# Kernel tuning notes

Hardware: AMD Instinct MI355X
Metric: run time of the kernel (lower is better)

The kernel has to match this reference:

```python
import jax, jax.numpy as jnp
import numpy as np

B, S, D = 8, 512, 1024
E, F, K = 8, 4096, 2


def setup_inputs() -> dict:
    key = jax.random.key(0)
    ks = jax.random.split(key, 8)
    scale = 1.0 / np.sqrt(D)
    return {
        "x": jax.random.normal(ks[0], (B, S, D), jnp.float32),
        "y": jax.random.randint(ks[1], (B,), 0, D),
        "W": jax.random.normal(ks[2], (D, D), jnp.float32) * scale,
        "b": jnp.zeros((D,), jnp.float32),
        "Wg": jax.random.normal(ks[3], (D, E), jnp.float32) * scale,
        "w1": jax.random.normal(ks[4], (E, D, F), jnp.float32) * scale,
        "b1": jnp.zeros((E, F), jnp.float32),
        "w2": jax.random.normal(ks[5], (E, F, D), jnp.float32) * (1.0 / np.sqrt(F)),
        "b2": jnp.zeros((E, D), jnp.float32),
    }


def reference(x, y, W, b, Wg, w1, b1, w2, b2):
    # linear projection (torch Linear convention: x @ W.T + b)
    lin = jnp.einsum("bsd,ed->bse", x, W) + b                      # [B,S,D]

    # --- MoE: top-2 softmax gate, renormalized over the top-k ---
    gate_logits = jnp.einsum("bsd,de->bse", lin, Wg)               # [B,S,E]
    probs = jax.nn.softmax(gate_logits, axis=-1)
    top_p, top_i = jax.lax.top_k(probs, K)                          # [B,S,K]
    top_p = top_p / jnp.sum(top_p, axis=-1, keepdims=True)
    # combine weights per expert: scatter top-k probs back to [B,S,E]
    gate = jnp.sum(jax.nn.one_hot(top_i, E, dtype=lin.dtype) * top_p[..., None], axis=-2)  # [B,S,E]

    # expert FFNs evaluated densely, combined by (sparse) gate weights
    h = jax.nn.relu(jnp.einsum("bsd,edf->ebsf", lin, w1) + b1[:, None, None, :])  # [E,B,S,F]
    expert_out = jnp.einsum("ebsf,efd->ebsd", h, w2) + b2[:, None, None, :]        # [E,B,S,D]
    moe_out = jnp.einsum("bse,ebsd->bsd", gate, expert_out)                        # [B,S,D]

    # residual, mean pool over sequence, cross-entropy
    sent_emb = jnp.mean(x + moe_out, axis=1)                       # [B,D] used as logits
    logp = jax.nn.log_softmax(sent_emb, axis=-1)
    loss = -jnp.mean(logp[jnp.arange(B), y])
    return loss
```

## Files before the change

kernel.cpp:

```cpp
#include <hip/hip_runtime.h>

#define TOK 4096
#define DD  1024
#define NE  8
#define FF  4096
#define NB  8
#define SS  512
#define HROWS 8320

typedef unsigned short ushort_t;
typedef __attribute__((ext_vector_type(8))) short bshort8;
typedef __attribute__((ext_vector_type(4))) float floatx4;

__device__ __forceinline__ ushort_t f2bf(float f) {
  unsigned int u = __float_as_uint(f);
  u += 0x7fffu + ((u >> 16) & 1u);
  return (ushort_t)(u >> 16);
}
__device__ __forceinline__ float bf2f(ushort_t h) {
  return __uint_as_float(((unsigned int)h) << 16);
}

__device__ __forceinline__ void gl_lds16(const ushort_t* g, ushort_t* l) {
  __builtin_amdgcn_global_load_lds(
      (const __attribute__((address_space(1))) unsigned int*)g,
      (__attribute__((address_space(3))) unsigned int*)l, 16, 0, 0);
}

__global__ __launch_bounds__(256) void k_cast(
    const float* __restrict__ in, ushort_t* __restrict__ out, int n4) {
  int i = blockIdx.x * 256 + threadIdx.x;
  if (i < n4) {
    float4 v = ((const float4*)in)[i];
    ushort4 o;
    o.x = f2bf(v.x); o.y = f2bf(v.y); o.z = f2bf(v.z); o.w = f2bf(v.w);
    ((ushort4*)out)[i] = o;
  }
}

__global__ __launch_bounds__(256) void k_transpose_cast(
    const float* __restrict__ in, size_t in_estride, int in_rstride,
    ushort_t* __restrict__ out, size_t out_estride, int out_rstride) {
  __shared__ ushort_t t[64][70];
  const float* ib = in + blockIdx.z * in_estride;
  ushort_t* ob = out + blockIdx.z * out_estride;
  const int r0 = blockIdx.y * 64, c0 = blockIdx.x * 64;
  const int tid = threadIdx.x;
  const int lr = tid >> 4, lc4 = (tid & 15) * 4;
#pragma unroll
  for (int it = 0; it < 4; ++it) {
    int r = lr + it * 16;
    float4 v = *(const float4*)&ib[(size_t)(r0 + r) * in_rstride + c0 + lc4];
    t[r][lc4 + 0] = f2bf(v.x);
    t[r][lc4 + 1] = f2bf(v.y);
    t[r][lc4 + 2] = f2bf(v.z);
    t[r][lc4 + 3] = f2bf(v.w);
  }
  __syncthreads();
  const int oc = tid >> 5, od2 = (tid & 31) * 2;
#pragma unroll
  for (int it = 0; it < 8; ++it) {
    int cc = oc + it * 8;
    ushort2 w;
    w.x = t[od2 + 0][cc];
    w.y = t[od2 + 1][cc];
    *(ushort2*)&ob[(size_t)(c0 + cc) * out_rstride + r0 + od2] = w;
  }
}

template <int MODE>
__global__ __launch_bounds__(256) void k_mfma(
    const ushort_t* __restrict__ A, const ushort_t* __restrict__ Bm,
    const float* __restrict__ bias, ushort_t* __restrict__ Obf,
    float* __restrict__ Of, const int* __restrict__ cnt,
    const int* __restrict__ offs, const int* __restrict__ btok, int f0,
    int accum, int kext, int ast, int ost, size_t bstride) {
  const int gx = gridDim.x, gy = gridDim.y;
  int flat = blockIdx.x + gx * (blockIdx.y + gy * blockIdx.z);
  const int nwg = gx * gy * (int)gridDim.z;
  flat = (flat & 7) * (nwg >> 3) + (flat >> 3);
  const int bx = flat % gx;
  const int t2 = flat / gx;
  const int by = t2 % gy;
  const int bz = t2 / gy;

  const int e = (MODE == 0) ? 0 : bz;
  int c = TOK, off = 0;
  if (MODE != 0) {
    c = cnt[e];
    off = offs[e];
    if (by * 128 >= c) return;
  }
  const int m0 = by * 128;
  const int n0 = bx * 128;
  const ushort_t* Bp = (MODE == 0) ? Bm : Bm + (size_t)e * bstride;

  __shared__ ushort_t Als[3][128 * 32];
  __shared__ ushort_t Bls[3][128 * 32];
  __shared__ int ts[128];

  const int tid = threadIdx.x;
  if (tid < 128) {
    int p = m0 + tid;
    int r;
    if (MODE == 0) r = p;
    else if (MODE == 1) r = btok[e * TOK + min(p, c - 1)];
    else r = off + p;
    ts[tid] = r;
  }
  __syncthreads();

  const int lane = tid & 63;
  const int w = tid >> 6;
  const int wm = (w & 1) * 64, wn = (w >> 1) * 64;
  const int lm = lane & 15, lq = lane >> 4;
  const int sr = lane >> 2;
  const int sg = lane & 3;

  const int r0 = w * 32 + sr;
  const int r1 = r0 + 16;
  const int q = (sg - (r0 >> 1)) & 3;
  const int d0 = r0 * 32 + sg * 8;
  const int d1 = r1 * 32 + sg * 8;
  const ushort_t* sA0 = A + (size_t)ts[r0] * ast + q * 8;
  const ushort_t* sA1 = A + (size_t)ts[r1] * ast + q * 8;
  const ushort_t* sB0 = Bp + (size_t)(n0 + r0) * kext + q * 8;
  const ushort_t* sB1 = Bp + (size_t)(n0 + r1) * kext + q * 8;

#define STG(bi, kt)                            \
  do {                                         \
    const int ko_ = (kt) << 5;                 \
    gl_lds16(sA0 + ko_, &Als[bi][d0]);         \
    gl_lds16(sA1 + ko_, &Als[bi][d1]);         \
    gl_lds16(sB0 + ko_, &Bls[bi][d0]);         \
    gl_lds16(sB1 + ko_, &Bls[bi][d1]);         \
  } while (0)

  floatx4 zero = {0.f, 0.f, 0.f, 0.f};
  floatx4 acc[4][4];
#pragma unroll
  for (int i = 0; i < 4; ++i)
#pragma unroll
    for (int j = 0; j < 4; ++j) acc[i][j] = zero;

  const int nk = kext >> 5;

  STG(0, 0);
  STG(1, 1);
  asm volatile("s_waitcnt vmcnt(4)" ::: "memory");
  asm volatile("s_barrier" ::: "memory");

  int cur = 0;
  for (int k = 0; k < nk; ++k) {
    const ushort_t* Ab = Als[cur];
    const ushort_t* Bb = Bls[cur];
    bshort8 af[4], bfr[4];
#pragma unroll
    for (int i = 0; i < 4; ++i) {
      int r = wm + i * 16 + lm;
      af[i] = *(const bshort8*)&Ab[r * 32 + (((lq + (r >> 1)) & 3) * 8)];
    }
#pragma unroll
    for (int j = 0; j < 4; ++j) {
      int r = wn + j * 16 + lm;
      bfr[j] = *(const bshort8*)&Bb[r * 32 + (((lq + (r >> 1)) & 3) * 8)];
    }
    int pf = cur + 2; if (pf >= 3) pf -= 3;
    if (k + 2 < nk) STG(pf, k + 2);

    asm volatile("s_waitcnt lgkmcnt(0)" ::: "memory");
    __builtin_amdgcn_sched_barrier(0);

#pragma unroll
    for (int i = 0; i < 4; ++i)
#pragma unroll
      for (int j = 0; j < 4; ++j)
        acc[i][j] = __builtin_amdgcn_mfma_f32_16x16x32_bf16(af[i], bfr[j],
                                                            acc[i][j], 0, 0, 0);

    if (k + 1 < nk) {
      if (k + 2 < nk) {
        asm volatile("s_waitcnt vmcnt(4)" ::: "memory");
      } else {
        asm volatile("s_waitcnt vmcnt(0)" ::: "memory");
      }
      asm volatile("s_barrier" ::: "memory");
    }
    cur += 1; if (cur >= 3) cur -= 3;
  }
#undef STG

#pragma unroll
  for (int i = 0; i < 4; ++i) {
#pragma unroll
    for (int j = 0; j < 4; ++j) {
      int n = wn + j * 16 + lm;
#pragma unroll
      for (int rr = 0; rr < 4; ++rr) {
        int m = wm + i * 16 + lq * 4 + rr;
        float v = acc[i][j][rr];
        if (MODE == 0) {
          int gn = n0 + n;
          v += bias[gn];
          Obf[(size_t)(m0 + m) * DD + gn] = f2bf(v);
        } else if (MODE == 1) {
          int p = m0 + m;
          if (p < c) {
            int gn = n0 + n;
            v += bias[(size_t)e * FF + f0 + gn];
            v = fmaxf(v, 0.f);
            Obf[(size_t)(off + p) * ost + gn] = f2bf(v);
          }
        } else {
          int p = m0 + m;
          if (p < c) {
            int gn = n0 + n;
            if (!accum) v += bias[(size_t)e * DD + gn];
            float* dp = &Of[(size_t)(off + p) * DD + gn];
            if (accum) *dp += v; else *dp = v;
          }
        }
      }
    }
  }
}

__global__ __launch_bounds__(256) void k_logits(
    const ushort_t* __restrict__ lin_bf, const float* __restrict__ Wg,
    int* __restrict__ topi, float* __restrict__ wts) {
  const int wv = threadIdx.x >> 6, lane = threadIdx.x & 63;
  const int t = blockIdx.x * 4 + wv;
  float acc[NE] = {};
  const ushort_t* lr = lin_bf + (size_t)t * DD;
#pragma unroll 4
  for (int d0 = 0; d0 < DD; d0 += 64) {
    float v = bf2f(lr[d0 + lane]);
    const float* wgr = Wg + (size_t)(d0 + lane) * NE;
    float4 g0 = *(const float4*)(wgr);
    float4 g1 = *(const float4*)(wgr + 4);
    acc[0] += v * g0.x; acc[1] += v * g0.y; acc[2] += v * g0.z; acc[3] += v * g0.w;
    acc[4] += v * g1.x; acc[5] += v * g1.y; acc[6] += v * g1.z; acc[7] += v * g1.w;
  }
#pragma unroll
  for (int off = 32; off > 0; off >>= 1) {
#pragma unroll
    for (int e = 0; e < NE; ++e) acc[e] += __shfl_xor(acc[e], off);
  }
  if (lane == 0) {
    int i1 = 0;
#pragma unroll
    for (int e = 1; e < NE; ++e)
      if (acc[e] > acc[i1]) i1 = e;
    int i2 = (i1 == 0) ? 1 : 0;
#pragma unroll
    for (int e = 0; e < NE; ++e)
      if (e != i1 && acc[e] > acc[i2]) i2 = e;
    float r = __expf(acc[i2] - acc[i1]);
    topi[t] = i1 | (i2 << 4);
    wts[2 * t + 0] = 1.0f / (1.0f + r);
    wts[2 * t + 1] = r / (1.0f + r);
  }
}

#define RT 512
__global__ __launch_bounds__(RT) void k_route(
    const int* __restrict__ topi, int* __restrict__ cnt, int* __restrict__ offs,
    int* __restrict__ btok, int* __restrict__ eslot) {
  __shared__ int sc[NE][RT + 1];
  __shared__ int tot[NE];
  const int tid = threadIdx.x;
  int lc[NE] = {};
  int my[8];
#pragma unroll
  for (int i = 0; i < 8; ++i) {
    int t = tid * 8 + i;
    int p = topi[t];
    my[i] = p;
    lc[p & 15]++;
    lc[(p >> 4) & 15]++;
  }
#pragma unroll
  for (int e = 0; e < NE; ++e) sc[e][tid] = lc[e];
  __syncthreads();
  if (tid < NE) {
    int s = 0;
    for (int i = 0; i < RT; ++i) { int v = sc[tid][i]; sc[tid][i] = s; s += v; }
    tot[tid] = s;
  }
  __syncthreads();
  if (tid == 0) {
    int s = 0;
    for (int e = 0; e < NE; ++e) { offs[e] = s; cnt[e] = tot[e]; s += tot[e]; }
  }
  __syncthreads();
  int run[NE];
#pragma unroll
  for (int e = 0; e < NE; ++e) run[e] = sc[e][tid];
#pragma unroll
  for (int i = 0; i < 8; ++i) {
    int t = tid * 8 + i, p = my[i];
    int e1 = p & 15, e2 = (p >> 4) & 15;
    int s1 = run[e1]++;
    btok[e1 * TOK + s1] = t;
    eslot[2 * t + 0] = e1 * TOK + s1;
    int s2 = run[e2]++;
    btok[e2 * TOK + s2] = t;
    eslot[2 * t + 1] = e2 * TOK + s2;
  }
}

__global__ __launch_bounds__(256) void k_pool(
    const float* __restrict__ x, const float* __restrict__ ob,
    const int* __restrict__ offs, const int* __restrict__ eslot,
    const float* __restrict__ wts, float* __restrict__ sent) {
  const int b = blockIdx.y;
  const int d = blockIdx.x * 256 + threadIdx.x;
  const int sc = blockIdx.z;
  float a = 0.f;
  for (int s = sc * 64; s < sc * 64 + 64; ++s) {
    int t = b * SS + s;
    int e0 = eslot[2 * t], e1 = eslot[2 * t + 1];
    int g0 = offs[e0 >> 12] + (e0 & (TOK - 1));
    int g1 = offs[e1 >> 12] + (e1 & (TOK - 1));
    a += x[(size_t)t * DD + d] + wts[2 * t] * ob[(size_t)g0 * DD + d] +
         wts[2 * t + 1] * ob[(size_t)g1 * DD + d];
  }
  atomicAdd(&sent[b * DD + d], a * (1.0f / SS));
}

__global__ __launch_bounds__(1024) void k_loss(
    const float* __restrict__ sent, const int* __restrict__ y,
    float* __restrict__ out) {
  __shared__ float red[16];
  const int tid = threadIdx.x;
  const int lane = tid & 63, wv = tid >> 6;
  float loss = 0.f;
  for (int b = 0; b < NB; ++b) {
    float v = sent[b * DD + tid];
    float m = v;
#pragma unroll
    for (int off = 32; off > 0; off >>= 1) m = fmaxf(m, __shfl_xor(m, off));
    if (lane == 0) red[wv] = m;
    __syncthreads();
    float m2 = red[0];
#pragma unroll
    for (int w = 1; w < 16; ++w) m2 = fmaxf(m2, red[w]);
    __syncthreads();
    float ex = __expf(v - m2);
#pragma unroll
    for (int off = 32; off > 0; off >>= 1) ex += __shfl_xor(ex, off);
    if (lane == 0) red[wv] = ex;
    __syncthreads();
    if (tid == 0) {
      float se = 0.f;
      for (int w = 0; w < 16; ++w) se += red[w];
      loss += m2 + logf(se) - sent[b * DD + y[b]];
    }
    __syncthreads();
  }
  if (tid == 0) out[0] = loss / NB;
}

extern "C" void kernel_launch(void* const* d_in, const int* in_sizes, int n_in,
                              void* d_out, int out_size, void* d_ws,
                              size_t ws_size, hipStream_t stream) {
  const float* x  = (const float*)d_in[0];
  const int*   y  = (const int*)d_in[1];
  const float* W  = (const float*)d_in[2];
  const float* bb = (const float*)d_in[3];
  const float* Wg = (const float*)d_in[4];
  const float* w1 = (const float*)d_in[5];
  const float* b1 = (const float*)d_in[6];
  const float* w2 = (const float*)d_in[7];
  const float* b2 = (const float*)d_in[8];
  float* out = (float*)d_out;

  auto need = [](size_t FCr) -> size_t {
    size_t o = 0;
    auto al = [&](size_t b) { o = (o + b + 255) & ~255ull; };
    al((size_t)TOK * DD * 2);
    al((size_t)TOK * DD * 2);
    al((size_t)DD * DD * 2);
    al((size_t)HROWS * FCr * 2);
    al((size_t)NE * FCr * DD * 2);
    al((size_t)NE * DD * FCr * 2);
    al((size_t)HROWS * DD * 4);
    al((size_t)NE * TOK * 4);
    al(64); al(64);
    al((size_t)TOK * 4);
    al((size_t)2 * TOK * 4);
    al((size_t)2 * TOK * 4);
    al((size_t)NB * DD * 4);
    return o;
  };
  const int nchunks = (ws_size >= need(FF)) ? 1 : 4;
  const int FCr = FF / nchunks;

  char* base = (char*)d_ws;
  size_t o = 0;
  auto al = [&](size_t b) -> char* {
    char* p = base + o;
    o = (o + b + 255) & ~255ull;
    return p;
  };
  ushort_t* lin_bf = (ushort_t*)al((size_t)TOK * DD * 2);
  ushort_t* x_bf   = (ushort_t*)al((size_t)TOK * DD * 2);
  ushort_t* W_bf   = (ushort_t*)al((size_t)DD * DD * 2);
  ushort_t* h_bf   = (ushort_t*)al((size_t)HROWS * FCr * 2);
  ushort_t* w1t    = (ushort_t*)al((size_t)NE * FCr * DD * 2);
  ushort_t* w2t    = (ushort_t*)al((size_t)NE * DD * FCr * 2);
  float*    ob     = (float*)al((size_t)HROWS * DD * 4);
  int*      btok   = (int*)al((size_t)NE * TOK * 4);
  int*      cnt    = (int*)al(64);
  int*      offs   = (int*)al(64);
  int*      topi   = (int*)al((size_t)TOK * 4);
  int*      eslot  = (int*)al((size_t)2 * TOK * 4);
  float*    wts    = (float*)al((size_t)2 * TOK * 4);
  float*    sent   = (float*)al((size_t)NB * DD * 4);

  hipMemsetAsync(sent, 0, NB * DD * sizeof(float), stream);

  k_cast<<<TOK * DD / 4 / 256, 256, 0, stream>>>(x, x_bf, TOK * DD / 4);
  k_cast<<<DD * DD / 4 / 256, 256, 0, stream>>>(W, W_bf, DD * DD / 4);

  k_mfma<0><<<dim3(DD / 128, TOK / 128), 256, 0, stream>>>(
      x_bf, W_bf, bb, lin_bf, nullptr, nullptr, nullptr, nullptr, 0, 0,
      DD, DD, DD, 0);

  k_logits<<<TOK / 4, 256, 0, stream>>>(lin_bf, Wg, topi, wts);
  k_route<<<1, RT, 0, stream>>>(topi, cnt, offs, btok, eslot);

  for (int ci = 0; ci < nchunks; ++ci) {
    int f0 = ci * FCr;
    k_transpose_cast<<<dim3(FCr / 64, DD / 64, NE), 256, 0, stream>>>(
        w1 + f0, (size_t)DD * FF, FF, w1t, (size_t)FCr * DD, DD);
    k_mfma<1><<<dim3(FCr / 128, TOK / 128, NE), 256, 0, stream>>>(
        lin_bf, w1t, b1, h_bf, nullptr, cnt, offs, btok, f0, 0,
        DD, DD, FCr, (size_t)FCr * DD);
    k_transpose_cast<<<dim3(DD / 64, FCr / 64, NE), 256, 0, stream>>>(
        w2 + (size_t)f0 * DD, (size_t)FF * DD, DD, w2t, (size_t)DD * FCr, FCr);
    k_mfma<2><<<dim3(DD / 128, TOK / 128, NE), 256, 0, stream>>>(
        h_bf, w2t, b2, nullptr, ob, cnt, offs, btok, f0, ci > 0 ? 1 : 0,
        FCr, FCr, DD, (size_t)DD * FCr);
  }

  k_pool<<<dim3(DD / 256, NB, 8), 256, 0, stream>>>(x, ob, offs, eslot, wts,
                                                    sent);
  k_loss<<<1, 1024, 0, stream>>>(sent, y, out);
}
```

Measured before the change: 613.3 us.

## Add large-tile 512-thread grouped GEMM kernel for MoE expert FFNs

Adds a k_mg kernel with 256-row M tiles, BK=64, XOR-swizzled LDS layout, double buffering, barrier-interleaved LDS fragment loads and MFMA with s_setprio, all run by 8 waves. The expert up- and down-projections now use it in place of the 128x128 k_mfma, which is reduced to the dense linear mode only. The aim is more operand reuse per tile and better overlap of loads with MFMA. In exchange it needs more LDS and registers per block, and per-expert tails waste more work with 256-row tiles.

```diff
diff --git a/kernel.cpp b/kernel.cpp
--- a/kernel.cpp
+++ b/kernel.cpp
@@ -82,34 +82,15 @@
   const int bx = flat % gx;
   const int t2 = flat / gx;
   const int by = t2 % gy;
-  const int bz = t2 / gy;
-
-  const int e = (MODE == 0) ? 0 : bz;
-  int c = TOK, off = 0;
-  if (MODE != 0) {
-    c = cnt[e];
-    off = offs[e];
-    if (by * 128 >= c) return;
-  }
+
   const int m0 = by * 128;
   const int n0 = bx * 128;
-  const ushort_t* Bp = (MODE == 0) ? Bm : Bm + (size_t)e * bstride;
+  const ushort_t* Bp = Bm;
 
   __shared__ ushort_t Als[3][128 * 32];
   __shared__ ushort_t Bls[3][128 * 32];
-  __shared__ int ts[128];
 
   const int tid = threadIdx.x;
-  if (tid < 128) {
-    int p = m0 + tid;
-    int r;
-    if (MODE == 0) r = p;
-    else if (MODE == 1) r = btok[e * TOK + min(p, c - 1)];
-    else r = off + p;
-    ts[tid] = r;
-  }
-  __syncthreads();
-
   const int lane = tid & 63;
   const int w = tid >> 6;
   const int wm = (w & 1) * 64, wn = (w >> 1) * 64;
@@ -122,8 +103,8 @@
   const int q = (sg - (r0 >> 1)) & 3;
   const int d0 = r0 * 32 + sg * 8;
   const int d1 = r1 * 32 + sg * 8;
-  const ushort_t* sA0 = A + (size_t)ts[r0] * ast + q * 8;
-  const ushort_t* sA1 = A + (size_t)ts[r1] * ast + q * 8;
+  const ushort_t* sA0 = A + (size_t)(m0 + r0) * ast + q * 8;
+  const ushort_t* sA1 = A + (size_t)(m0 + r1) * ast + q * 8;
   const ushort_t* sB0 = Bp + (size_t)(n0 + r0) * kext + q * 8;
   const ushort_t* sB1 = Bp + (size_t)(n0 + r1) * kext + q * 8;
 
@@ -199,22 +180,184 @@
       for (int rr = 0; rr < 4; ++rr) {
         int m = wm + i * 16 + lq * 4 + rr;
         float v = acc[i][j][rr];
-        if (MODE == 0) {
-          int gn = n0 + n;
-          v += bias[gn];
-          Obf[(size_t)(m0 + m) * DD + gn] = f2bf(v);
-        } else if (MODE == 1) {
-          int p = m0 + m;
-          if (p < c) {
-            int gn = n0 + n;
+        int gn = n0 + n;
+        v += bias[gn];
+        Obf[(size_t)(m0 + m) * DD + gn] = f2bf(v);
+      }
+    }
+  }
+}
+
+template <int MODE, int BN>
+__global__ __launch_bounds__(512, 2) void k_mg(
+    const ushort_t* __restrict__ A, const ushort_t* __restrict__ Bm,
+    const float* __restrict__ bias, ushort_t* __restrict__ Obf,
+    float* __restrict__ Of, const int* __restrict__ cnt,
+    const int* __restrict__ offs, const int* __restrict__ btok, int f0,
+    int accum, int kext, int ast, int ost, size_t bstride) {
+  constexpr int NFR = BN / 64;
+  constexpr int NLB = BN / 64;
+  constexpr int VM = 4 + NLB;
+
+  const int gx = gridDim.x, gy = gridDim.y;
+  int flat = blockIdx.x + gx * (blockIdx.y + gy * blockIdx.z);
+  const int nwg = gx * gy * (int)gridDim.z;
+  flat = (flat & 7) * (nwg >> 3) + (flat >> 3);
+  const int bx = flat % gx;
+  const int t2 = flat / gx;
+  const int by = t2 % gy;
+  const int bz = t2 / gy;
+
+  const int e = bz;
+  const int c = cnt[e];
+  const int off = offs[e];
+  if (by * 256 >= c) return;
+  const int m0 = by * 256;
+  const int n0 = bx * BN;
+  const ushort_t* Bp = Bm + (size_t)e * bstride;
+
+  __shared__ ushort_t Als[2][256 * 64];
+  __shared__ ushort_t Bls[2][BN * 64];
+  __shared__ int ts[256];
+
+  const int tid = threadIdx.x;
+  if (tid < 256) {
+    int p = m0 + tid;
+    int r;
+    if (MODE == 1) r = btok[e * TOK + min(p, c - 1)];
+    else r = off + min(p, c - 1);
+    ts[tid] = r;
+  }
+  __syncthreads();
+
+  const int lane = tid & 63;
+  const int w = tid >> 6;
+  const int wmi = w >> 2, wni = w & 3;
+  const int wm = wmi * 128;
+  const int wn = wni * (BN / 4);
+  const int lm = lane & 15, lq = lane >> 4;
+
+  const int srow = lane >> 3;
+  const int sq = (lane & 7) ^ srow;
+  const ushort_t* sAp[4];
+  const ushort_t* sBp[NLB];
+#pragma unroll
+  for (int i = 0; i < 4; ++i)
+    sAp[i] = A + (size_t)ts[i * 64 + w * 8 + srow] * ast + sq * 8;
+#pragma unroll
+  for (int i = 0; i < NLB; ++i)
+    sBp[i] = Bp + (size_t)(n0 + i * 64 + w * 8 + srow) * kext + sq * 8;
+
+#define STAGE(bi, kt)                                                   \
+  do {                                                                  \
+    const int ko_ = (kt) * 64;                                          \
+    _Pragma("unroll") for (int i_ = 0; i_ < 4; ++i_)                    \
+        gl_lds16(sAp[i_] + ko_,                                         \
+                 &Als[bi][(i_ * 64 + w * 8) * 64 + lane * 8]);          \
+    _Pragma("unroll") for (int i_ = 0; i_ < NLB; ++i_)                  \
+        gl_lds16(sBp[i_] + ko_,                                         \
+                 &Bls[bi][(i_ * 64 + w * 8) * 64 + lane * 8]);          \
+  } while (0)
+
+#define LDA_(MH)                                                        \
+  _Pragma("unroll") for (int f_ = 0; f_ < 4; ++f_) {                    \
+    const int r_ = wm + (MH)*64 + f_ * 16 + lm;                         \
+    _Pragma("unroll") for (int s_ = 0; s_ < 2; ++s_)                    \
+        aF[f_][s_] = *(const bshort8*)&Ab[r_ * 64 +                     \
+            (((s_ * 4 + lq) ^ (r_ & 7)) * 8)];                          \
+  }
+#define LDB_(N0)                                                        \
+  _Pragma("unroll") for (int j_ = 0; j_ < 2; ++j_) {                    \
+    const int r_ = wn + ((N0) + j_) * 16 + lm;                          \
+    _Pragma("unroll") for (int s_ = 0; s_ < 2; ++s_)                    \
+        bF[j_][s_] = *(const bshort8*)&Bb[r_ * 64 +                     \
+            (((s_ * 4 + lq) ^ (r_ & 7)) * 8)];                          \
+  }
+#define MM_(MH, N0)                                                     \
+  __builtin_amdgcn_s_setprio(1);                                        \
+  _Pragma("unroll") for (int f_ = 0; f_ < 4; ++f_)                      \
+  _Pragma("unroll") for (int j_ = 0; j_ < 2; ++j_)                      \
+  _Pragma("unroll") for (int s_ = 0; s_ < 2; ++s_)                      \
+      acc[(MH)*4 + f_][(N0) + j_] = __builtin_amdgcn_mfma_f32_16x16x32_bf16( \
+          aF[f_][s_], bF[j_][s_], acc[(MH)*4 + f_][(N0) + j_], 0, 0, 0); \
+  __builtin_amdgcn_s_setprio(0);
+
+  floatx4 acc[8][NFR];
+#pragma unroll
+  for (int i = 0; i < 8; ++i)
+#pragma unroll
+    for (int j = 0; j < NFR; ++j) acc[i][j] = (floatx4){0.f, 0.f, 0.f, 0.f};
+
+  const int NT = kext / 64;
+
+  STAGE(0, 0);
+  STAGE(1, 1);
+  if constexpr (VM == 8) asm volatile("s_waitcnt vmcnt(8)" ::: "memory");
+  else asm volatile("s_waitcnt vmcnt(6)" ::: "memory");
+  __builtin_amdgcn_s_barrier();
+
+  for (int kt = 0; kt < NT; ++kt) {
+    const int buf = kt & 1;
+    const ushort_t* Ab = Als[buf];
+    const ushort_t* Bb = Bls[buf];
+    bshort8 aF[4][2], bF[2][2];
+
+    if constexpr (NFR == 4) {
+      LDA_(0); LDB_(0);
+      __builtin_amdgcn_s_barrier();
+      MM_(0, 0);
+      LDB_(2);
+      __builtin_amdgcn_s_barrier();
+      MM_(0, 2);
+      LDA_(1);
+      __builtin_amdgcn_s_barrier();
+      MM_(1, 2);
+      LDB_(0);
+      __builtin_amdgcn_s_barrier();
+      MM_(1, 0);
+    } else {
+      LDA_(0); LDB_(0);
+      __builtin_amdgcn_s_barrier();
+      MM_(0, 0);
+      LDA_(1);
+      __builtin_amdgcn_s_barrier();
+      MM_(1, 0);
+    }
+
+    __builtin_amdgcn_s_barrier();
+    if (kt + 2 < NT) STAGE(buf, kt + 2);
+    if (kt + 1 < NT) {
+      if (kt + 2 < NT) {
+        if constexpr (VM == 8) asm volatile("s_waitcnt vmcnt(8)" ::: "memory");
+        else asm volatile("s_waitcnt vmcnt(6)" ::: "memory");
+      } else {
+        asm volatile("s_waitcnt vmcnt(0)" ::: "memory");
+      }
+      __builtin_amdgcn_s_barrier();
+    }
+  }
+#undef STAGE
+#undef LDA_
+#undef LDB_
+#undef MM_
+
+#pragma unroll
+  for (int mf = 0; mf < 8; ++mf) {
+#pragma unroll
+    for (int nf = 0; nf < NFR; ++nf) {
+      const int n = wn + nf * 16 + lm;
+#pragma unroll
+      for (int rr = 0; rr < 4; ++rr) {
+        const int m = wm + mf * 16 + lq * 4 + rr;
+        float v = acc[mf][nf][rr];
+        const int p = m0 + m;
+        if (p < c) {
+          const int gn = n0 + n;
+          if (MODE == 1) {
             v += bias[(size_t)e * FF + f0 + gn];
             v = fmaxf(v, 0.f);
             Obf[(size_t)(off + p) * ost + gn] = f2bf(v);
-          }
-        } else {
-          int p = m0 + m;
-          if (p < c) {
-            int gn = n0 + n;
+          } else {
             if (!accum) v += bias[(size_t)e * DD + gn];
             float* dp = &Of[(size_t)(off + p) * DD + gn];
             if (accum) *dp += v; else *dp = v;
@@ -434,12 +577,12 @@
     int f0 = ci * FCr;
     k_transpose_cast<<<dim3(FCr / 64, DD / 64, NE), 256, 0, stream>>>(
         w1 + f0, (size_t)DD * FF, FF, w1t, (size_t)FCr * DD, DD);
-    k_mfma<1><<<dim3(FCr / 128, TOK / 128, NE), 256, 0, stream>>>(
+    k_mg<1, 256><<<dim3(FCr / 256, TOK / 256, NE), 512, 0, stream>>>(
         lin_bf, w1t, b1, h_bf, nullptr, cnt, offs, btok, f0, 0,
         DD, DD, FCr, (size_t)FCr * DD);
     k_transpose_cast<<<dim3(DD / 64, FCr / 64, NE), 256, 0, stream>>>(
         w2 + (size_t)f0 * DD, (size_t)FF * DD, DD, w2t, (size_t)DD * FCr, FCr);
-    k_mfma<2><<<dim3(DD / 128, TOK / 128, NE), 256, 0, stream>>>(
+    k_mg<2, 128><<<dim3(DD / 128, TOK / 256, NE), 512, 0, stream>>>(
         h_bf, w2t, b2, nullptr, ob, cnt, offs, btok, f0, ci > 0 ? 1 : 0,
         FCr, FCr, DD, (size_t)DD * FCr);
   }
```

Result: slower. 746.5 us (+21.7%).

## Use 256x128 tiles with 512-thread blocks for grouped expert GEMMs

Applied to the files above, without the earlier changes.

The grouped expert GEMMs (modes 1 and 2) now use 512-thread workgroups computing 256x128 output tiles, with 8 waves each owning a 64x64 subtile. Each B tile loaded to LDS is reused across twice as many rows, and the staging is rebalanced to three loads per thread. The dense projection GEMM is split out into its own specialised non-template kernel. The larger M tile wastes more work on expert row counts that are not multiples of 256, and the bigger LDS footprint may lower occupancy.

```diff
diff --git a/kernel.cpp b/kernel.cpp
--- a/kernel.cpp
+++ b/kernel.cpp
@@ -68,8 +68,122 @@
   }
 }
 
+__global__ __launch_bounds__(256) void k_mfma0(
+    const ushort_t* __restrict__ A, const ushort_t* __restrict__ Bm,
+    const float* __restrict__ bias, ushort_t* __restrict__ Obf, int kext) {
+  const int gx = gridDim.x, gy = gridDim.y;
+  int flat = blockIdx.x + gx * blockIdx.y;
+  const int nwg = gx * gy;
+  flat = (flat & 7) * (nwg >> 3) + (flat >> 3);
+  const int bx = flat % gx;
+  const int by = flat / gx;
+
+  const int m0 = by * 128;
+  const int n0 = bx * 128;
+
+  __shared__ ushort_t Als[3][128 * 32];
+  __shared__ ushort_t Bls[3][128 * 32];
+
+  const int tid = threadIdx.x;
+  const int lane = tid & 63;
+  const int w = tid >> 6;
+  const int wm = (w & 1) * 64, wn = (w >> 1) * 64;
+  const int lm = lane & 15, lq = lane >> 4;
+  const int sr = lane >> 2;
+  const int sg = lane & 3;
+
+  const int r0 = w * 32 + sr;
+  const int r1 = r0 + 16;
+  const int q = (sg - (r0 >> 1)) & 3;
+  const int d0 = r0 * 32 + sg * 8;
+  const int d1 = r1 * 32 + sg * 8;
+  const ushort_t* sA0 = A + (size_t)(m0 + r0) * kext + q * 8;
+  const ushort_t* sA1 = A + (size_t)(m0 + r1) * kext + q * 8;
+  const ushort_t* sB0 = Bm + (size_t)(n0 + r0) * kext + q * 8;
+  const ushort_t* sB1 = Bm + (size_t)(n0 + r1) * kext + q * 8;
+
+#define STG0(bi, kt)                           \
+  do {                                         \
+    const int ko_ = (kt) << 5;                 \
+    gl_lds16(sA0 + ko_, &Als[bi][d0]);         \
+    gl_lds16(sA1 + ko_, &Als[bi][d1]);         \
+    gl_lds16(sB0 + ko_, &Bls[bi][d0]);         \
+    gl_lds16(sB1 + ko_, &Bls[bi][d1]);         \
+  } while (0)
+
+  floatx4 zero = {0.f, 0.f, 0.f, 0.f};
+  floatx4 acc[4][4];
+#pragma unroll
+  for (int i = 0; i < 4; ++i)
+#pragma unroll
+    for (int j = 0; j < 4; ++j) acc[i][j] = zero;
+
+  const int nk = kext >> 5;
+
+  STG0(0, 0);
+  STG0(1, 1);
+  asm volatile("s_waitcnt vmcnt(4)" ::: "memory");
+  asm volatile("s_barrier" ::: "memory");
+
+  int cur = 0;
+  for (int k = 0; k < nk; ++k) {
+    const ushort_t* Ab = Als[cur];
+    const ushort_t* Bb = Bls[cur];
+    bshort8 af[4], bfr[4];
+#pragma unroll
+    for (int i = 0; i < 4; ++i) {
+      int r = wm + i * 16 + lm;
+      af[i] = *(const bshort8*)&Ab[r * 32 + (((lq + (r >> 1)) & 3) * 8)];
+    }
+#pragma unroll
+    for (int j = 0; j < 4; ++j) {
+      int r = wn + j * 16 + lm;
+      bfr[j] = *(const bshort8*)&Bb[r * 32 + (((lq + (r >> 1)) & 3) * 8)];
+    }
+    int pf = cur + 2; if (pf >= 3) pf -= 3;
+    if (k + 2 < nk) STG0(pf, k + 2);
+
+    asm volatile("s_waitcnt lgkmcnt(0)" ::: "memory");
+    __builtin_amdgcn_sched_barrier(0);
+
+#pragma unroll
+    for (int i = 0; i < 4; ++i)
+#pragma unroll
+      for (int j = 0; j < 4; ++j)
+        acc[i][j] = __builtin_amdgcn_mfma_f32_16x16x32_bf16(af[i], bfr[j],
+                                                            acc[i][j], 0, 0, 0);
+
+    if (k + 1 < nk) {
+      if (k + 2 < nk) {
+        asm volatile("s_waitcnt vmcnt(4)" ::: "memory");
+      } else {
+        asm volatile("s_waitcnt vmcnt(0)" ::: "memory");
+      }
+      asm volatile("s_barrier" ::: "memory");
+    }
+    cur += 1; if (cur >= 3) cur -= 3;
+  }
+#undef STG0
+
+#pragma unroll
+  for (int i = 0; i < 4; ++i) {
+#pragma unroll
+    for (int j = 0; j < 4; ++j) {
+      int n = wn + j * 16 + lm;
+#pragma unroll
+      for (int rr = 0; rr < 4; ++rr) {
+        int m = wm + i * 16 + lq * 4 + rr;
+        float v = acc[i][j][rr];
+        int gn = n0 + n;
+        v += bias[gn];
+        Obf[(size_t)(m0 + m) * DD + gn] = f2bf(v);
+      }
+    }
+  }
+}
+
 template <int MODE>
-__global__ __launch_bounds__(256) void k_mfma(
+__global__ __launch_bounds__(512, 4) void k_mg(
     const ushort_t* __restrict__ A, const ushort_t* __restrict__ Bm,
     const float* __restrict__ bias, ushort_t* __restrict__ Obf,
     float* __restrict__ Of, const int* __restrict__ cnt,
@@ -84,56 +198,51 @@
   const int by = t2 % gy;
   const int bz = t2 / gy;
 
-  const int e = (MODE == 0) ? 0 : bz;
-  int c = TOK, off = 0;
-  if (MODE != 0) {
-    c = cnt[e];
-    off = offs[e];
-    if (by * 128 >= c) return;
-  }
-  const int m0 = by * 128;
+  const int e = bz;
+  const int c = cnt[e];
+  const int off = offs[e];
+  if (by * 256 >= c) return;
+  const int m0 = by * 256;
   const int n0 = bx * 128;
-  const ushort_t* Bp = (MODE == 0) ? Bm : Bm + (size_t)e * bstride;
-
-  __shared__ ushort_t Als[3][128 * 32];
+  const ushort_t* Bp = Bm + (size_t)e * bstride;
+
+  __shared__ ushort_t Als[3][256 * 32];
   __shared__ ushort_t Bls[3][128 * 32];
-  __shared__ int ts[128];
+  __shared__ int ts[256];
 
   const int tid = threadIdx.x;
-  if (tid < 128) {
+  if (tid < 256) {
     int p = m0 + tid;
     int r;
-    if (MODE == 0) r = p;
-    else if (MODE == 1) r = btok[e * TOK + min(p, c - 1)];
-    else r = off + p;
+    if (MODE == 1) r = btok[e * TOK + min(p, c - 1)];
+    else r = off + min(p, c - 1);
     ts[tid] = r;
   }
   __syncthreads();
 
   const int lane = tid & 63;
   const int w = tid >> 6;
-  const int wm = (w & 1) * 64, wn = (w >> 1) * 64;
+  const int wm = (w >> 1) * 64;
+  const int wn = (w & 1) * 64;
   const int lm = lane & 15, lq = lane >> 4;
   const int sr = lane >> 2;
   const int sg = lane & 3;
 
-  const int r0 = w * 32 + sr;
-  const int r1 = r0 + 16;
-  const int q = (sg - (r0 >> 1)) & 3;
-  const int d0 = r0 * 32 + sg * 8;
-  const int d1 = r1 * 32 + sg * 8;
-  const ushort_t* sA0 = A + (size_t)ts[r0] * ast + q * 8;
-  const ushort_t* sA1 = A + (size_t)ts[r1] * ast + q * 8;
-  const ushort_t* sB0 = Bp + (size_t)(n0 + r0) * kext + q * 8;
-  const ushort_t* sB1 = Bp + (size_t)(n0 + r1) * kext + q * 8;
+  const int ra0 = w * 16 + sr;
+  const int ra1 = 128 + ra0;
+  const int q = (sg - (ra0 >> 1)) & 3;
+  const int dA0 = ra0 * 32 + sg * 8;
+  const int dA1 = ra1 * 32 + sg * 8;
+  const ushort_t* sA0 = A + (size_t)ts[ra0] * ast + q * 8;
+  const ushort_t* sA1 = A + (size_t)ts[ra1] * ast + q * 8;
+  const ushort_t* sB0 = Bp + (size_t)(n0 + ra0) * kext + q * 8;
 
 #define STG(bi, kt)                            \
   do {                                         \
     const int ko_ = (kt) << 5;                 \
-    gl_lds16(sA0 + ko_, &Als[bi][d0]);         \
-    gl_lds16(sA1 + ko_, &Als[bi][d1]);         \
-    gl_lds16(sB0 + ko_, &Bls[bi][d0]);         \
-    gl_lds16(sB1 + ko_, &Bls[bi][d1]);         \
+    gl_lds16(sA0 + ko_, &Als[bi][dA0]);        \
+    gl_lds16(sA1 + ko_, &Als[bi][dA1]);        \
+    gl_lds16(sB0 + ko_, &Bls[bi][dA0]);        \
   } while (0)
 
   floatx4 zero = {0.f, 0.f, 0.f, 0.f};
@@ -147,7 +256,7 @@
 
   STG(0, 0);
   STG(1, 1);
-  asm volatile("s_waitcnt vmcnt(4)" ::: "memory");
+  asm volatile("s_waitcnt vmcnt(3)" ::: "memory");
   asm volatile("s_barrier" ::: "memory");
 
   int cur = 0;
@@ -180,7 +289,7 @@
 
     if (k + 1 < nk) {
       if (k + 2 < nk) {
-        asm volatile("s_waitcnt vmcnt(4)" ::: "memory");
+        asm volatile("s_waitcnt vmcnt(3)" ::: "memory");
       } else {
         asm volatile("s_waitcnt vmcnt(0)" ::: "memory");
       }
@@ -194,27 +303,19 @@
   for (int i = 0; i < 4; ++i) {
 #pragma unroll
     for (int j = 0; j < 4; ++j) {
-      int n = wn + j * 16 + lm;
+      const int n = wn + j * 16 + lm;
 #pragma unroll
       for (int rr = 0; rr < 4; ++rr) {
-        int m = wm + i * 16 + lq * 4 + rr;
+        const int m = wm + i * 16 + lq * 4 + rr;
         float v = acc[i][j][rr];
-        if (MODE == 0) {
-          int gn = n0 + n;
-          v += bias[gn];
-          Obf[(size_t)(m0 + m) * DD + gn] = f2bf(v);
-        } else if (MODE == 1) {
-          int p = m0 + m;
-          if (p < c) {
-            int gn = n0 + n;
+        const int p = m0 + m;
+        if (p < c) {
+          const int gn = n0 + n;
+          if (MODE == 1) {
             v += bias[(size_t)e * FF + f0 + gn];
             v = fmaxf(v, 0.f);
             Obf[(size_t)(off + p) * ost + gn] = f2bf(v);
-          }
-        } else {
-          int p = m0 + m;
-          if (p < c) {
-            int gn = n0 + n;
+          } else {
             if (!accum) v += bias[(size_t)e * DD + gn];
             float* dp = &Of[(size_t)(off + p) * DD + gn];
             if (accum) *dp += v; else *dp = v;
@@ -423,9 +524,8 @@
   k_cast<<<TOK * DD / 4 / 256, 256, 0, stream>>>(x, x_bf, TOK * DD / 4);
   k_cast<<<DD * DD / 4 / 256, 256, 0, stream>>>(W, W_bf, DD * DD / 4);
 
-  k_mfma<0><<<dim3(DD / 128, TOK / 128), 256, 0, stream>>>(
-      x_bf, W_bf, bb, lin_bf, nullptr, nullptr, nullptr, nullptr, 0, 0,
-      DD, DD, DD, 0);
+  k_mfma0<<<dim3(DD / 128, TOK / 128), 256, 0, stream>>>(
+      x_bf, W_bf, bb, lin_bf, DD);
 
   k_logits<<<TOK / 4, 256, 0, stream>>>(lin_bf, Wg, topi, wts);
   k_route<<<1, RT, 0, stream>>>(topi, cnt, offs, btok, eslot);
@@ -434,12 +534,12 @@
     int f0 = ci * FCr;
     k_transpose_cast<<<dim3(FCr / 64, DD / 64, NE), 256, 0, stream>>>(
         w1 + f0, (size_t)DD * FF, FF, w1t, (size_t)FCr * DD, DD);
-    k_mfma<1><<<dim3(FCr / 128, TOK / 128, NE), 256, 0, stream>>>(
+    k_mg<1><<<dim3(FCr / 128, TOK / 256, NE), 512, 0, stream>>>(
         lin_bf, w1t, b1, h_bf, nullptr, cnt, offs, btok, f0, 0,
         DD, DD, FCr, (size_t)FCr * DD);
     k_transpose_cast<<<dim3(DD / 64, FCr / 64, NE), 256, 0, stream>>>(
         w2 + (size_t)f0 * DD, (size_t)FF * DD, DD, w2t, (size_t)DD * FCr, FCr);
-    k_mfma<2><<<dim3(DD / 128, TOK / 128, NE), 256, 0, stream>>>(
+    k_mg<2><<<dim3(DD / 128, TOK / 256, NE), 512, 0, stream>>>(
         h_bf, w2t, b2, nullptr, ob, cnt, offs, btok, f0, ci > 0 ? 1 : 0,
         FCr, FCr, DD, (size_t)DD * FCr);
   }
```

New measurement: 599.8 us. 1.02x faster.
